# Performance work log

Hardware: AMD Instinct MI355X
Metric: run time of the kernel (lower is better)

The kernel has to match this reference:

```python
import jax, jax.numpy as jnp
import numpy as np

M, N, DV, DC, ITERS = 512, 1024, 3, 6, 10
BATCH = 8192
ATANH_CLIP = 0.999995


def _build_graph():
    """Deterministic (3,6)-regular Tanner graph, edge order = row-major nonzeros of H."""
    offsets = [0, 1, 2, 512, 515, 519]
    H = np.zeros((M, N), np.int64)
    r = np.arange(M)
    for off in offsets:
        H[r, (2 * r + off) % N] = 1
    ei, ej = np.nonzero(H)                       # E = M*DC = 3072 edges, row-major
    E = ei.size
    var2edges = np.argsort(ej, kind='stable').reshape(N, DV)   # edges of each variable
    chk2edges = np.argsort(ei, kind='stable').reshape(M, DC)   # edges of each check
    v_sum = np.empty((E, DV - 1), np.int64)      # for edge e: other edges on same variable
    c_prod = np.empty((E, DC - 1), np.int64)     # for edge e: other edges on same check
    for e in range(E):
        gv = var2edges[ej[e]]
        v_sum[e] = gv[gv != e]
        gc = chk2edges[ei[e]]
        c_prod[e] = gc[gc != e]
    return v_sum, c_prod, ej.astype(np.int64), var2edges


def setup_inputs() -> dict:
    key = jax.random.key(0)
    ks = jax.random.split(key, 6)
    v_sum, c_prod, edge_var, var2edges = _build_graph()
    E = edge_var.shape[0]                        # 3072
    TW = E * (DV - 1)                            # total_weights = 6144
    return {
        "llr": jax.random.normal(ks[0], (BATCH, N), jnp.float32),
        "w_iter": 1.0 + 0.1 * jax.random.normal(ks[1], (ITERS, TW), jnp.float32),
        "llr_iter": 1.0 + 0.1 * jax.random.normal(ks[2], (ITERS, N), jnp.float32),
        "w_final": 1.0 + 0.1 * jax.random.normal(ks[3], (E,), jnp.float32),
        "llr_final": 1.0 + 0.1 * jax.random.normal(ks[4], (N,), jnp.float32),
        "v_sum_idx": jnp.asarray(v_sum),         # [E, DV-1]
        "c_prod_idx": jnp.asarray(c_prod),       # [E, DC-1]
        "edge_var": jnp.asarray(edge_var),       # [E] variable index of each edge
        "final_idx": jnp.asarray(var2edges),     # [N, DV] edges feeding each variable marginal
    }


def reference(llr, w_iter, llr_iter, w_final, llr_final,
              v_sum_idx, c_prod_idx, edge_var, final_idx):
    B = llr.shape[0]
    E = edge_var.shape[0]
    c2v0 = jnp.zeros((B, E), llr.dtype)

    def bp_iter(c2v, params):
        w, lw = params                                      # [E*(DV-1)], [N]
        # variable -> check: weighted sum of extrinsic c2v messages + weighted LLR
        s = (c2v[:, v_sum_idx] * w.reshape(E, DV - 1)).sum(-1)        # [B,E]
        v2c = jnp.tanh(0.5 * (s + (llr * lw)[:, edge_var]))           # [B,E]
        # check -> variable: product of extrinsic v2c messages, 2*atanh
        prods = v2c[:, c_prod_idx].prod(-1)                           # [B,E]
        return 2.0 * jnp.arctanh(ATANH_CLIP * prods), None

    c2v, _ = jax.lax.scan(bp_iter, c2v0, (w_iter, llr_iter))
    # final marginalization: per-variable sum of weighted incoming messages
    fin = (c2v[:, final_idx.reshape(-1)] * w_final).reshape(B, N, DV).sum(-1)
    out = fin + llr * llr_final
    return jax.nn.sigmoid(out[:, : N - M])
```

## Files before the change

### kernel.cpp

```cpp
#include <hip/hip_runtime.h>


namespace {

typedef float v4f __attribute__((ext_vector_type(4)));

constexpr int T      = 512;
constexpr int ROWS   = 4;
constexpr int EEDG   = 3072;
constexpr int NVAR   = 1024;
constexpr int NITER  = 10;
constexpr int BATCH  = 8192;
constexpr int NOUT   = 512;

constexpr float LOG2E = 1.4426950408889634f;
constexpr float LN2   = 0.6931471805599453f;
constexpr float KAPPA = 0.999995f;
constexpr float ACLMP = 24.0f;

__device__ __forceinline__ float fast_exp2(float x) { return __builtin_amdgcn_exp2f(x); }
__device__ __forceinline__ float fast_log2(float x) { return __builtin_amdgcn_logf(x); }
__device__ __forceinline__ float fast_rcp (float x) { return __builtin_amdgcn_rcpf(x); }

__global__ __launch_bounds__(T, 2)
void bp_decode(const float* __restrict__ llr,
               const float* __restrict__ w_iter,
               const float* __restrict__ llr_iter,
               const float* __restrict__ w_final,
               const float* __restrict__ llr_final,
               const int*  __restrict__ v_sum_idx,
               const int*  __restrict__ edge_var,
               const int*  __restrict__ final_idx,
               float* __restrict__ out)
{
    __shared__ v4f Ad[EEDG];

    const int  tid = threadIdx.x;
    const long b0  = (long)blockIdx.x * ROWS;

    #pragma unroll
    for (int k = 0; k < 6; ++k)
        Ad[k * T + tid] = (v4f)(0.f);

    unsigned nbp[6];
    unsigned varp[3];
    v4f      Lpre[6];
    {
        const int4* p = (const int4*)(v_sum_idx + 12 * tid);
        int4 q0 = p[0], q1 = p[1], q2 = p[2];
        nbp[0] = (unsigned)q0.x | ((unsigned)q0.y << 16);
        nbp[1] = (unsigned)q0.z | ((unsigned)q0.w << 16);
        nbp[2] = (unsigned)q1.x | ((unsigned)q1.y << 16);
        nbp[3] = (unsigned)q1.z | ((unsigned)q1.w << 16);
        nbp[4] = (unsigned)q2.x | ((unsigned)q2.y << 16);
        nbp[5] = (unsigned)q2.z | ((unsigned)q2.w << 16);
    }
    {
        int var[6];
        const int2* p = (const int2*)(edge_var + 6 * tid);
        int2 q0 = p[0], q1 = p[1], q2 = p[2];
        var[0]=q0.x; var[1]=q0.y; var[2]=q1.x; var[3]=q1.y; var[4]=q2.x; var[5]=q2.y;
        #pragma unroll
        for (int i = 0; i < 3; ++i)
            varp[i] = (unsigned)var[2*i] | ((unsigned)var[2*i+1] << 16);
        #pragma unroll
        for (int j = 0; j < 6; ++j) {
            v4f L;
            L.x = llr[(b0 + 0) * NVAR + var[j]];
            L.y = llr[(b0 + 1) * NVAR + var[j]];
            L.z = llr[(b0 + 2) * NVAR + var[j]];
            L.w = llr[(b0 + 3) * NVAR + var[j]];
            Lpre[j] = L * LOG2E;
        }
    }

    const int own = 6 * tid;

    float w[12], lv[6];
    {
        const float* p = w_iter + 12 * tid;
        float4 a = ((const float4*)p)[0], b = ((const float4*)p)[1], c = ((const float4*)p)[2];
        w[0]=a.x; w[1]=a.y; w[2]=a.z;  w[3]=a.w;
        w[4]=b.x; w[5]=b.y; w[6]=b.z;  w[7]=b.w;
        w[8]=c.x; w[9]=c.y; w[10]=c.z; w[11]=c.w;
        #pragma unroll
        for (int i = 0; i < 3; ++i) {
            unsigned q = varp[i];
            lv[2*i]   = llr_iter[q & 0xffffu];
            lv[2*i+1] = llr_iter[q >> 16];
        }
    }

    __syncthreads();

    #pragma unroll 2
    for (int it = 0; it < NITER; ++it) {
        v4f a[6];
        #pragma unroll
        for (int j = 0; j < 6; ++j) a[j] = Lpre[j] * lv[j];
        #pragma unroll
        for (int i = 0; i < 6; ++i) {
            unsigned p  = nbp[i];
            v4f ga = Ad[p & 0xffffu];
            v4f gb = Ad[p >> 16];
            a[i] = a[i] + w[2*i] * ga + w[2*i+1] * gb;
        }

        __syncthreads();

        {
            const int itn = (it + 1 < NITER) ? it + 1 : it;
            const float* p = w_iter + itn * (EEDG * 2) + 12 * tid;
            float4 qa = ((const float4*)p)[0], qb = ((const float4*)p)[1], qc = ((const float4*)p)[2];
            const float* lit = llr_iter + itn * NVAR;
            float lvn[6];
            #pragma unroll
            for (int i = 0; i < 3; ++i) {
                unsigned q = varp[i];
                lvn[2*i]   = lit[q & 0xffffu];
                lvn[2*i+1] = lit[q >> 16];
            }

            v4f zm[6], zp[6];
            #pragma unroll
            for (int j = 0; j < 6; ++j) {
                v4f aa = __builtin_elementwise_min(a[j], (v4f)(ACLMP));
                v4f z;
                z.x = fast_exp2(aa.x);
                z.y = fast_exp2(aa.y);
                z.z = fast_exp2(aa.z);
                z.w = fast_exp2(aa.w);
                zm[j] = z - 1.f;
                zp[j] = z + 1.f;
            }
            v4f A[6], B[6];
            {
                v4f P1=zm[0], P2=P1*zm[1], P3=P2*zm[2], P4=P3*zm[3], P5=P4*zm[4];
                v4f S4=zm[5], S3=S4*zm[4], S2=S3*zm[3], S1=S2*zm[2], S0=S1*zm[1];
                A[0]=S0; A[1]=P1*S1; A[2]=P2*S2; A[3]=P3*S3; A[4]=P4*S4; A[5]=P5;
            }
            {
                v4f P1=zp[0], P2=P1*zp[1], P3=P2*zp[2], P4=P3*zp[3], P5=P4*zp[4];
                v4f S4=zp[5], S3=S4*zp[4], S2=S3*zp[3], S1=S2*zp[2], S0=S1*zp[1];
                B[0]=S0; B[1]=P1*S1; B[2]=P2*S2; B[3]=P3*S3; B[4]=P4*S4; B[5]=P5;
            }
            #pragma unroll
            for (int j = 0; j < 6; ++j) {
                v4f num = KAPPA * A[j] + B[j];
                v4f den = B[j] - KAPPA * A[j];
                v4f d;
                d.x = fast_log2(num.x) - fast_log2(den.x);
                d.y = fast_log2(num.y) - fast_log2(den.y);
                d.z = fast_log2(num.z) - fast_log2(den.z);
                d.w = fast_log2(num.w) - fast_log2(den.w);
                Ad[own + j] = d;
            }

            w[0]=qa.x; w[1]=qa.y; w[2]=qa.z;  w[3]=qa.w;
            w[4]=qb.x; w[5]=qb.y; w[6]=qb.z;  w[7]=qb.w;
            w[8]=qc.x; w[9]=qc.y; w[10]=qc.z; w[11]=qc.w;
            #pragma unroll
            for (int j = 0; j < 6; ++j) lv[j] = lvn[j];
        }

        __syncthreads();
    }

    {
        int f0 = final_idx[3*tid], f1 = final_idx[3*tid + 1], f2 = final_idx[3*tid + 2];
        v4f d0 = Ad[f0];
        v4f d1 = Ad[f1];
        v4f d2 = Ad[f2];
        float wf0 = w_final[3*tid], wf1 = w_final[3*tid + 1], wf2 = w_final[3*tid + 2];
        float lf  = llr_final[tid];
        v4f l;
        l.x = llr[(b0 + 0) * NVAR + tid];
        l.y = llr[(b0 + 1) * NVAR + tid];
        l.z = llr[(b0 + 2) * NVAR + tid];
        l.w = llr[(b0 + 3) * NVAR + tid];

        v4f fin = (d0 * wf0 + d1 * wf1 + d2 * wf2) * LN2;
        v4f v   = l * lf + fin;
        out[(b0 + 0) * NOUT + tid] = fast_rcp(1.f + fast_exp2(-v.x * LOG2E));
        out[(b0 + 1) * NOUT + tid] = fast_rcp(1.f + fast_exp2(-v.y * LOG2E));
        out[(b0 + 2) * NOUT + tid] = fast_rcp(1.f + fast_exp2(-v.z * LOG2E));
        out[(b0 + 3) * NOUT + tid] = fast_rcp(1.f + fast_exp2(-v.w * LOG2E));
    }
}

}

extern "C" void kernel_launch(void* const* d_in, const int* in_sizes, int n_in,
                              void* d_out, int out_size, void* d_ws, size_t ws_size,
                              hipStream_t stream)
{
    const float* llr       = (const float*)d_in[0];
    const float* w_iter    = (const float*)d_in[1];
    const float* llr_iter  = (const float*)d_in[2];
    const float* w_final   = (const float*)d_in[3];
    const float* llr_final = (const float*)d_in[4];
    const int*   v_sum_idx = (const int*)d_in[5];
    const int*   edge_var  = (const int*)d_in[7];
    const int*   final_idx = (const int*)d_in[8];
    float* outp = (float*)d_out;

    dim3 grid(BATCH / ROWS), block(T);
    hipLaunchKernelGGL(bp_decode, grid, block, 0, stream,
                       llr, w_iter, llr_iter, w_final, llr_final,
                       v_sum_idx, edge_var, final_idx, outp);
}
```

Baseline: 212.4 us.

## Halve rows per block, swizzle shared message layout, raise occupancy target

Each block now decodes two batch rows instead of four, so the shared message array holds float2 instead of float4 (24 KB instead of 48 KB) and registers per thread shrink. The launch bound is raised to 8 blocks per CU to get more resident waves that can hide LDS and transcendental latency. A bit-swizzle on edge indices remaps where each thread's six owned messages are stored, meant to cut LDS bank conflicts on the strided stores and gathers. The trade-off is twice as many blocks, each repeating the per-thread index and weight loads, and a possibly tighter register budget.

Result: slower. 463.9 us (+118.4%).

```diff
diff --git a/kernel.cpp b/kernel.cpp
--- a/kernel.cpp
+++ b/kernel.cpp
@@ -3,10 +3,10 @@
 
 namespace {
 
-typedef float v4f __attribute__((ext_vector_type(4)));
+typedef float v2f __attribute__((ext_vector_type(2)));
 
 constexpr int T      = 512;
-constexpr int ROWS   = 4;
+constexpr int ROWS   = 2;
 constexpr int EEDG   = 3072;
 constexpr int NVAR   = 1024;
 constexpr int NITER  = 10;
@@ -22,7 +22,11 @@
 __device__ __forceinline__ float fast_log2(float x) { return __builtin_amdgcn_logf(x); }
 __device__ __forceinline__ float fast_rcp (float x) { return __builtin_amdgcn_rcpf(x); }
 
-__global__ __launch_bounds__(T, 2)
+__device__ __forceinline__ int swz(int s) {
+    return (s & ~31) | ((s >> 1) & 15) | ((s & 1) << 4);
+}
+
+__global__ __launch_bounds__(T, 8)
 void bp_decode(const float* __restrict__ llr,
                const float* __restrict__ w_iter,
                const float* __restrict__ llr_iter,
@@ -33,28 +37,31 @@
                const int*  __restrict__ final_idx,
                float* __restrict__ out)
 {
-    __shared__ v4f Ad[EEDG];
+    __shared__ v2f Ad[EEDG];
 
     const int  tid = threadIdx.x;
     const long b0  = (long)blockIdx.x * ROWS;
 
     #pragma unroll
     for (int k = 0; k < 6; ++k)
-        Ad[k * T + tid] = (v4f)(0.f);
+        Ad[k * T + tid] = (v2f)(0.f);
 
     unsigned nbp[6];
     unsigned varp[3];
-    v4f      Lpre[6];
+    v2f      Lpre[6];
+    int      ows[6];
     {
         const int4* p = (const int4*)(v_sum_idx + 12 * tid);
         int4 q0 = p[0], q1 = p[1], q2 = p[2];
-        nbp[0] = (unsigned)q0.x | ((unsigned)q0.y << 16);
-        nbp[1] = (unsigned)q0.z | ((unsigned)q0.w << 16);
-        nbp[2] = (unsigned)q1.x | ((unsigned)q1.y << 16);
-        nbp[3] = (unsigned)q1.z | ((unsigned)q1.w << 16);
-        nbp[4] = (unsigned)q2.x | ((unsigned)q2.y << 16);
-        nbp[5] = (unsigned)q2.z | ((unsigned)q2.w << 16);
-    }
+        nbp[0] = (unsigned)swz(q0.x) | ((unsigned)swz(q0.y) << 16);
+        nbp[1] = (unsigned)swz(q0.z) | ((unsigned)swz(q0.w) << 16);
+        nbp[2] = (unsigned)swz(q1.x) | ((unsigned)swz(q1.y) << 16);
+        nbp[3] = (unsigned)swz(q1.z) | ((unsigned)swz(q1.w) << 16);
+        nbp[4] = (unsigned)swz(q2.x) | ((unsigned)swz(q2.y) << 16);
+        nbp[5] = (unsigned)swz(q2.z) | ((unsigned)swz(q2.w) << 16);
+    }
+    #pragma unroll
+    for (int j = 0; j < 6; ++j) ows[j] = swz(6 * tid + j);
     {
         int var[6];
         const int2* p = (const int2*)(edge_var + 6 * tid);
@@ -65,16 +72,12 @@
             varp[i] = (unsigned)var[2*i] | ((unsigned)var[2*i+1] << 16);
         #pragma unroll
         for (int j = 0; j < 6; ++j) {
-            v4f L;
+            v2f L;
             L.x = llr[(b0 + 0) * NVAR + var[j]];
             L.y = llr[(b0 + 1) * NVAR + var[j]];
-            L.z = llr[(b0 + 2) * NVAR + var[j]];
-            L.w = llr[(b0 + 3) * NVAR + var[j]];
             Lpre[j] = L * LOG2E;
         }
     }
-
-    const int own = 6 * tid;
 
     float w[12], lv[6];
     {
@@ -95,14 +98,14 @@
 
     #pragma unroll 2
     for (int it = 0; it < NITER; ++it) {
-        v4f a[6];
+        v2f a[6];
         #pragma unroll
         for (int j = 0; j < 6; ++j) a[j] = Lpre[j] * lv[j];
         #pragma unroll
         for (int i = 0; i < 6; ++i) {
             unsigned p  = nbp[i];
-            v4f ga = Ad[p & 0xffffu];
-            v4f gb = Ad[p >> 16];
+            v2f ga = Ad[p & 0xffffu];
+            v2f gb = Ad[p >> 16];
             a[i] = a[i] + w[2*i] * ga + w[2*i+1] * gb;
         }
 
@@ -121,39 +124,35 @@
                 lvn[2*i+1] = lit[q >> 16];
             }
 
-            v4f zm[6], zp[6];
+            v2f zm[6], zp[6];
             #pragma unroll
             for (int j = 0; j < 6; ++j) {
-                v4f aa = __builtin_elementwise_min(a[j], (v4f)(ACLMP));
-                v4f z;
+                v2f aa = __builtin_elementwise_min(a[j], (v2f)(ACLMP));
+                v2f z;
                 z.x = fast_exp2(aa.x);
                 z.y = fast_exp2(aa.y);
-                z.z = fast_exp2(aa.z);
-                z.w = fast_exp2(aa.w);
                 zm[j] = z - 1.f;
                 zp[j] = z + 1.f;
             }
-            v4f A[6], B[6];
+            v2f A[6], B[6];
             {
-                v4f P1=zm[0], P2=P1*zm[1], P3=P2*zm[2], P4=P3*zm[3], P5=P4*zm[4];
-                v4f S4=zm[5], S3=S4*zm[4], S2=S3*zm[3], S1=S2*zm[2], S0=S1*zm[1];
+                v2f P1=zm[0], P2=P1*zm[1], P3=P2*zm[2], P4=P3*zm[3], P5=P4*zm[4];
+                v2f S4=zm[5], S3=S4*zm[4], S2=S3*zm[3], S1=S2*zm[2], S0=S1*zm[1];
                 A[0]=S0; A[1]=P1*S1; A[2]=P2*S2; A[3]=P3*S3; A[4]=P4*S4; A[5]=P5;
             }
             {
-                v4f P1=zp[0], P2=P1*zp[1], P3=P2*zp[2], P4=P3*zp[3], P5=P4*zp[4];
-                v4f S4=zp[5], S3=S4*zp[4], S2=S3*zp[3], S1=S2*zp[2], S0=S1*zp[1];
+                v2f P1=zp[0], P2=P1*zp[1], P3=P2*zp[2], P4=P3*zp[3], P5=P4*zp[4];
+                v2f S4=zp[5], S3=S4*zp[4], S2=S3*zp[3], S1=S2*zp[2], S0=S1*zp[1];
                 B[0]=S0; B[1]=P1*S1; B[2]=P2*S2; B[3]=P3*S3; B[4]=P4*S4; B[5]=P5;
             }
             #pragma unroll
             for (int j = 0; j < 6; ++j) {
-                v4f num = KAPPA * A[j] + B[j];
-                v4f den = B[j] - KAPPA * A[j];
-                v4f d;
+                v2f num = KAPPA * A[j] + B[j];
+                v2f den = B[j] - KAPPA * A[j];
+                v2f d;
                 d.x = fast_log2(num.x) - fast_log2(den.x);
                 d.y = fast_log2(num.y) - fast_log2(den.y);
-                d.z = fast_log2(num.z) - fast_log2(den.z);
-                d.w = fast_log2(num.w) - fast_log2(den.w);
-                Ad[own + j] = d;
+                Ad[ows[j]] = d;
             }
 
             w[0]=qa.x; w[1]=qa.y; w[2]=qa.z;  w[3]=qa.w;
@@ -167,24 +166,20 @@
     }
 
     {
-        int f0 = final_idx[3*tid], f1 = final_idx[3*tid + 1], f2 = final_idx[3*tid + 2];
-        v4f d0 = Ad[f0];
-        v4f d1 = Ad[f1];
-        v4f d2 = Ad[f2];
+        int f0 = swz(final_idx[3*tid]), f1 = swz(final_idx[3*tid + 1]), f2 = swz(final_idx[3*tid + 2]);
+        v2f d0 = Ad[f0];
+        v2f d1 = Ad[f1];
+        v2f d2 = Ad[f2];
         float wf0 = w_final[3*tid], wf1 = w_final[3*tid + 1], wf2 = w_final[3*tid + 2];
         float lf  = llr_final[tid];
-        v4f l;
+        v2f l;
         l.x = llr[(b0 + 0) * NVAR + tid];
         l.y = llr[(b0 + 1) * NVAR + tid];
-        l.z = llr[(b0 + 2) * NVAR + tid];
-        l.w = llr[(b0 + 3) * NVAR + tid];
-
-        v4f fin = (d0 * wf0 + d1 * wf1 + d2 * wf2) * LN2;
-        v4f v   = l * lf + fin;
+
+        v2f fin = (d0 * wf0 + d1 * wf1 + d2 * wf2) * LN2;
+        v2f v   = l * lf + fin;
         out[(b0 + 0) * NOUT + tid] = fast_rcp(1.f + fast_exp2(-v.x * LOG2E));
         out[(b0 + 1) * NOUT + tid] = fast_rcp(1.f + fast_exp2(-v.y * LOG2E));
-        out[(b0 + 2) * NOUT + tid] = fast_rcp(1.f + fast_exp2(-v.z * LOG2E));
-        out[(b0 + 3) * NOUT + tid] = fast_rcp(1.f + fast_exp2(-v.w * LOG2E));
     }
 }
 
```

## Double-buffer LDS messages, swizzle edge indices, drop a barrier per iteration

Applied to the files above, without the earlier changes.

Shared memory holds two copies of the per-edge message array, so each iteration reads one buffer and writes the other. That removes the barrier between the gather phase and the write-back phase, leaving one barrier per iteration. Edge indices are swizzled to spread each thread's six consecutive v4f stores and the gathers across LDS banks, and launch bounds drop to one block per SIMD pair because LDS usage doubles to 96KB. The cost is halved occupancy, which may reduce latency hiding, plus more registers for the unpacked index arrays.

Result: slower. 236.3 us (+11.3%).

```diff
diff --git a/kernel.cpp b/kernel.cpp
--- a/kernel.cpp
+++ b/kernel.cpp
@@ -22,7 +22,11 @@
 __device__ __forceinline__ float fast_log2(float x) { return __builtin_amdgcn_logf(x); }
 __device__ __forceinline__ float fast_rcp (float x) { return __builtin_amdgcn_rcpf(x); }
 
-__global__ __launch_bounds__(T, 2)
+__device__ __forceinline__ int swz(int s) {
+    return (s & ~31) | ((s >> 1) & 15) | ((s & 1) << 4);
+}
+
+__global__ __launch_bounds__(T, 1)
 void bp_decode(const float* __restrict__ llr,
                const float* __restrict__ w_iter,
                const float* __restrict__ llr_iter,
@@ -33,7 +37,7 @@
                const int*  __restrict__ final_idx,
                float* __restrict__ out)
 {
-    __shared__ v4f Ad[EEDG];
+    __shared__ v4f Ad[2 * EEDG];
 
     const int  tid = threadIdx.x;
     const long b0  = (long)blockIdx.x * ROWS;
@@ -42,27 +46,23 @@
     for (int k = 0; k < 6; ++k)
         Ad[k * T + tid] = (v4f)(0.f);
 
-    unsigned nbp[6];
-    unsigned varp[3];
-    v4f      Lpre[6];
+    int nb[12];
+    int own[6];
+    int var[6];
+    v4f Lpre[6];
     {
         const int4* p = (const int4*)(v_sum_idx + 12 * tid);
         int4 q0 = p[0], q1 = p[1], q2 = p[2];
-        nbp[0] = (unsigned)q0.x | ((unsigned)q0.y << 16);
-        nbp[1] = (unsigned)q0.z | ((unsigned)q0.w << 16);
-        nbp[2] = (unsigned)q1.x | ((unsigned)q1.y << 16);
-        nbp[3] = (unsigned)q1.z | ((unsigned)q1.w << 16);
-        nbp[4] = (unsigned)q2.x | ((unsigned)q2.y << 16);
-        nbp[5] = (unsigned)q2.z | ((unsigned)q2.w << 16);
-    }
-    {
-        int var[6];
+        nb[0]  = swz(q0.x); nb[1]  = swz(q0.y); nb[2]  = swz(q0.z); nb[3]  = swz(q0.w);
+        nb[4]  = swz(q1.x); nb[5]  = swz(q1.y); nb[6]  = swz(q1.z); nb[7]  = swz(q1.w);
+        nb[8]  = swz(q2.x); nb[9]  = swz(q2.y); nb[10] = swz(q2.z); nb[11] = swz(q2.w);
+    }
+    #pragma unroll
+    for (int j = 0; j < 6; ++j) own[j] = swz(6 * tid + j);
+    {
         const int2* p = (const int2*)(edge_var + 6 * tid);
         int2 q0 = p[0], q1 = p[1], q2 = p[2];
         var[0]=q0.x; var[1]=q0.y; var[2]=q1.x; var[3]=q1.y; var[4]=q2.x; var[5]=q2.y;
-        #pragma unroll
-        for (int i = 0; i < 3; ++i)
-            varp[i] = (unsigned)var[2*i] | ((unsigned)var[2*i+1] << 16);
         #pragma unroll
         for (int j = 0; j < 6; ++j) {
             v4f L;
@@ -74,8 +74,6 @@
         }
     }
 
-    const int own = 6 * tid;
-
     float w[12], lv[6];
     {
         const float* p = w_iter + 12 * tid;
@@ -84,90 +82,83 @@
         w[4]=b.x; w[5]=b.y; w[6]=b.z;  w[7]=b.w;
         w[8]=c.x; w[9]=c.y; w[10]=c.z; w[11]=c.w;
         #pragma unroll
-        for (int i = 0; i < 3; ++i) {
-            unsigned q = varp[i];
-            lv[2*i]   = llr_iter[q & 0xffffu];
-            lv[2*i+1] = llr_iter[q >> 16];
-        }
+        for (int j = 0; j < 6; ++j) lv[j] = llr_iter[var[j]];
     }
 
     __syncthreads();
 
-    #pragma unroll 2
-    for (int it = 0; it < NITER; ++it) {
-        v4f a[6];
-        #pragma unroll
-        for (int j = 0; j < 6; ++j) a[j] = Lpre[j] * lv[j];
-        #pragma unroll
-        for (int i = 0; i < 6; ++i) {
-            unsigned p  = nbp[i];
-            v4f ga = Ad[p & 0xffffu];
-            v4f gb = Ad[p >> 16];
-            a[i] = a[i] + w[2*i] * ga + w[2*i+1] * gb;
-        }
-
-        __syncthreads();
-
-        {
-            const int itn = (it + 1 < NITER) ? it + 1 : it;
-            const float* p = w_iter + itn * (EEDG * 2) + 12 * tid;
-            float4 qa = ((const float4*)p)[0], qb = ((const float4*)p)[1], qc = ((const float4*)p)[2];
-            const float* lit = llr_iter + itn * NVAR;
-            float lvn[6];
-            #pragma unroll
-            for (int i = 0; i < 3; ++i) {
-                unsigned q = varp[i];
-                lvn[2*i]   = lit[q & 0xffffu];
-                lvn[2*i+1] = lit[q >> 16];
-            }
-
-            v4f zm[6], zp[6];
-            #pragma unroll
-            for (int j = 0; j < 6; ++j) {
-                v4f aa = __builtin_elementwise_min(a[j], (v4f)(ACLMP));
-                v4f z;
-                z.x = fast_exp2(aa.x);
-                z.y = fast_exp2(aa.y);
-                z.z = fast_exp2(aa.z);
-                z.w = fast_exp2(aa.w);
-                zm[j] = z - 1.f;
-                zp[j] = z + 1.f;
-            }
-            v4f A[6], B[6];
-            {
-                v4f P1=zm[0], P2=P1*zm[1], P3=P2*zm[2], P4=P3*zm[3], P5=P4*zm[4];
-                v4f S4=zm[5], S3=S4*zm[4], S2=S3*zm[3], S1=S2*zm[2], S0=S1*zm[1];
-                A[0]=S0; A[1]=P1*S1; A[2]=P2*S2; A[3]=P3*S3; A[4]=P4*S4; A[5]=P5;
-            }
-            {
-                v4f P1=zp[0], P2=P1*zp[1], P3=P2*zp[2], P4=P3*zp[3], P5=P4*zp[4];
-                v4f S4=zp[5], S3=S4*zp[4], S2=S3*zp[3], S1=S2*zp[2], S0=S1*zp[1];
-                B[0]=S0; B[1]=P1*S1; B[2]=P2*S2; B[3]=P3*S3; B[4]=P4*S4; B[5]=P5;
-            }
-            #pragma unroll
-            for (int j = 0; j < 6; ++j) {
-                v4f num = KAPPA * A[j] + B[j];
-                v4f den = B[j] - KAPPA * A[j];
-                v4f d;
-                d.x = fast_log2(num.x) - fast_log2(den.x);
-                d.y = fast_log2(num.y) - fast_log2(den.y);
-                d.z = fast_log2(num.z) - fast_log2(den.z);
-                d.w = fast_log2(num.w) - fast_log2(den.w);
-                Ad[own + j] = d;
-            }
-
-            w[0]=qa.x; w[1]=qa.y; w[2]=qa.z;  w[3]=qa.w;
-            w[4]=qb.x; w[5]=qb.y; w[6]=qb.z;  w[7]=qb.w;
-            w[8]=qc.x; w[9]=qc.y; w[10]=qc.z; w[11]=qc.w;
-            #pragma unroll
-            for (int j = 0; j < 6; ++j) lv[j] = lvn[j];
-        }
-
-        __syncthreads();
-    }
-
-    {
-        int f0 = final_idx[3*tid], f1 = final_idx[3*tid + 1], f2 = final_idx[3*tid + 2];
+#define BP_ITER(IT, RDOFF, WROFF) do {                                          \
+        v4f a_[6];                                                              \
+        _Pragma("unroll")                                                       \
+        for (int j = 0; j < 6; ++j) a_[j] = Lpre[j] * lv[j];                    \
+        _Pragma("unroll")                                                       \
+        for (int i = 0; i < 6; ++i) {                                           \
+            v4f ga = Ad[nb[2*i]   + (RDOFF)];                 \
+            v4f gb = Ad[nb[2*i+1] + (RDOFF)];                                   \
+            a_[i] = a_[i] + w[2*i] * ga + w[2*i+1] * gb;                        \
+        }                                                                       \
+             \
+        const int itn_ = ((IT) + 1 < NITER) ? (IT) + 1 : (IT);                  \
+        const float* pw_ = w_iter + (long)itn_ * (EEDG * 2) + 12 * tid;         \
+        float4 qa_ = ((const float4*)pw_)[0];                                   \
+        float4 qb_ = ((const float4*)pw_)[1];                                   \
+        float4 qc_ = ((const float4*)pw_)[2];                                   \
+        const float* lit_ = llr_iter + itn_ * NVAR;                             \
+        float lvn_[6];                                                          \
+        _Pragma("unroll")                                                       \
+        for (int j = 0; j < 6; ++j) lvn_[j] = lit_[var[j]];                     \
+                                                     \
+        v4f zm_[6], zp_[6];                                                     \
+        _Pragma("unroll")                                                       \
+        for (int j = 0; j < 6; ++j) {                                           \
+            v4f aa = __builtin_elementwise_min(a_[j], (v4f)(ACLMP));            \
+            v4f z;                                                              \
+            z.x = fast_exp2(aa.x);                                              \
+            z.y = fast_exp2(aa.y);                                              \
+            z.z = fast_exp2(aa.z);                                              \
+            z.w = fast_exp2(aa.w);                                              \
+            zm_[j] = z - 1.f;                                                   \
+            zp_[j] = z + 1.f;                                                   \
+        }                                                                       \
+        v4f A_[6], B_[6];                                                       \
+        {                                                                       \
+            v4f P1=zm_[0], P2=P1*zm_[1], P3=P2*zm_[2], P4=P3*zm_[3], P5=P4*zm_[4]; \
+            v4f S4=zm_[5], S3=S4*zm_[4], S2=S3*zm_[3], S1=S2*zm_[2], S0=S1*zm_[1]; \
+            A_[0]=S0; A_[1]=P1*S1; A_[2]=P2*S2; A_[3]=P3*S3; A_[4]=P4*S4; A_[5]=P5; \
+        }                                                                       \
+        {                                                                       \
+            v4f P1=zp_[0], P2=P1*zp_[1], P3=P2*zp_[2], P4=P3*zp_[3], P5=P4*zp_[4]; \
+            v4f S4=zp_[5], S3=S4*zp_[4], S2=S3*zp_[3], S1=S2*zp_[2], S0=S1*zp_[1]; \
+            B_[0]=S0; B_[1]=P1*S1; B_[2]=P2*S2; B_[3]=P3*S3; B_[4]=P4*S4; B_[5]=P5; \
+        }                                                                       \
+        _Pragma("unroll")                                                       \
+        for (int j = 0; j < 6; ++j) {                                           \
+            v4f num = KAPPA * A_[j] + B_[j];                        \
+            v4f den = B_[j] - KAPPA * A_[j];                        \
+            v4f d;                                                              \
+            d.x = fast_log2(num.x) - fast_log2(den.x);                          \
+            d.y = fast_log2(num.y) - fast_log2(den.y);                          \
+            d.z = fast_log2(num.z) - fast_log2(den.z);                          \
+            d.w = fast_log2(num.w) - fast_log2(den.w);                          \
+            Ad[own[j] + (WROFF)] = d;                        \
+        }                                                                       \
+                                     \
+        w[0]=qa_.x; w[1]=qa_.y; w[2]=qa_.z;  w[3]=qa_.w;                        \
+        w[4]=qb_.x; w[5]=qb_.y; w[6]=qb_.z;  w[7]=qb_.w;                        \
+        w[8]=qc_.x; w[9]=qc_.y; w[10]=qc_.z; w[11]=qc_.w;                       \
+        _Pragma("unroll")                                                       \
+        for (int j = 0; j < 6; ++j) lv[j] = lvn_[j];                            \
+        __syncthreads();                                                        \
+    } while (0)
+
+    for (int it = 0; it < NITER; it += 2) {
+        BP_ITER(it,     0,    EEDG);
+        BP_ITER(it + 1, EEDG, 0);
+    }
+#undef BP_ITER
+
+    {
+        int f0 = swz(final_idx[3*tid]), f1 = swz(final_idx[3*tid + 1]), f2 = swz(final_idx[3*tid + 2]);
         v4f d0 = Ad[f0];
         v4f d1 = Ad[f1];
         v4f d2 = Ad[f2];
```
